# Kernel optimization log

Measured on AMD Instinct MI355X. Metric: run time of the kernel, lower is better.

## Reference

```python
import jax, jax.numpy as jnp
import numpy as np

B, D, S, H = 16384, 512, 3, 8
HD = D // H


def setup_inputs() -> dict:
    key = jax.random.key(0)
    ks = jax.random.split(key, 12)
    n = lambda k, shp, s=0.02: jax.random.normal(k, shp, jnp.float32) * s
    return {
        'x': jax.random.normal(ks[0], (B, D), jnp.float32),
        'h_prev': jax.random.normal(ks[1], (S, B, D), jnp.float32),
        'c_prev': jax.random.normal(ks[2], (S, B, D), jnp.float32),
        'ssm_state': jax.random.normal(ks[3], (B, D), jnp.float32),
        'Wt': n(ks[4], (S, D, D)),          # per-scale transform Linear weight
        'bt': jnp.zeros((S, D), jnp.float32),
        'ln_g': jnp.ones((S, D), jnp.float32),
        'ln_b': jnp.zeros((S, D), jnp.float32),
        'W_ih': n(ks[5], (S, 4 * D, D)),    # LSTMCell input weights (i,f,g,o)
        'W_hh': n(ks[6], (S, 4 * D, D)),
        'b_ih': jnp.zeros((S, 4 * D), jnp.float32),
        'b_hh': jnp.zeros((S, 4 * D), jnp.float32),
        'decays': jnp.linspace(0.5, 0.9, S, dtype=jnp.float32),
        'in_proj_w': n(ks[7], (3 * D, D)),  # MHA packed q/k/v projections
        'in_proj_b': jnp.zeros((3 * D,), jnp.float32),
        'out_proj_w': n(ks[8], (D, D)),
        'out_proj_b': jnp.zeros((D,), jnp.float32),
        'mix_w': n(ks[9], (D, S * D)),
        'mix_b': jnp.zeros((D,), jnp.float32),
    }


def reference(x, h_prev, c_prev, ssm_state, Wt, bt, ln_g, ln_b,
              W_ih, W_hh, b_ih, b_hh, decays,
              in_proj_w, in_proj_b, out_proj_w, out_proj_b, mix_w, mix_b):
    # per-scale transform: Linear -> LayerNorm -> exact GELU  (S,B,D)
    xs = jnp.einsum('bd,sed->sbe', x, Wt) + bt[:, None, :]
    mu = xs.mean(-1, keepdims=True)
    var = ((xs - mu) ** 2).mean(-1, keepdims=True)
    xs = (xs - mu) * jax.lax.rsqrt(var + 1e-5) * ln_g[:, None, :] + ln_b[:, None, :]
    xs = jax.nn.gelu(xs, approximate=False)
    # LSTMCell (all scales vectorized); gate order i,f,g,o as in torch
    gates = (jnp.einsum('sbe,sge->sbg', xs, W_ih) + b_ih[:, None, :]
             + jnp.einsum('sbd,sgd->sbg', h_prev, W_hh) + b_hh[:, None, :])
    ig, fg, gg, og = jnp.split(gates, 4, axis=-1)
    c_lstm = jax.nn.sigmoid(fg) * c_prev + jax.nn.sigmoid(ig) * jnp.tanh(gg)
    h_new = jax.nn.sigmoid(og) * jnp.tanh(c_lstm)
    d = decays[:, None, None]
    c_new = d * c_prev + (1.0 - d) * c_lstm  # decay blend (h uses pre-blend c)
    # torch.cat(outputs, dim=-1): scale-major feature blocks  (B, S*D)
    multi = jnp.transpose(h_new, (1, 0, 2)).reshape(B, S * D)
    # MHA fusion: query = ssm_state (1 token), keys/values = scale outputs
    Wq, Wk, Wv = jnp.split(in_proj_w, 3, axis=0)
    bq, bk, bv = jnp.split(in_proj_b, 3)
    q = (ssm_state @ Wq.T + bq).reshape(B, H, HD)
    k = (jnp.einsum('sbd,ed->sbe', h_new, Wk) + bk).reshape(S, B, H, HD)
    v = (jnp.einsum('sbd,ed->sbe', h_new, Wv) + bv).reshape(S, B, H, HD)
    scale = jnp.float32(1.0 / np.sqrt(HD))
    attn = jax.nn.softmax(jnp.einsum('bhd,sbhd->bhs', q, k) * scale, axis=-1)
    fused = jnp.einsum('bhs,sbhd->bhd', attn, v).reshape(B, D) @ out_proj_w.T + out_proj_b
    out = multi @ mix_w.T + mix_b + fused
    return out, h_new, c_new
```

## Files before the change

### kernel.cpp

```cpp
#include <hip/hip_runtime.h>
#include <stdint.h>


#define Bq 16384
#define Dq 512
#define Sq 3
#define Hq 8

typedef unsigned short u16;
typedef __bf16 bf16x8 __attribute__((ext_vector_type(8)));
typedef float f32x4 __attribute__((ext_vector_type(4)));
typedef u16 u16x8 __attribute__((ext_vector_type(8)));
typedef u16 u16x4v __attribute__((ext_vector_type(4)));

__device__ __forceinline__ u16 f2bf(float f) {
    union { float f; uint32_t u; } c; c.f = f;
    uint32_t u = c.u;
    return (u16)((u + 0x7fffu + ((u >> 16) & 1u)) >> 16);
}
__device__ __forceinline__ float bf2f(u16 h) {
    union { uint32_t u; float f; } c; c.u = ((uint32_t)h) << 16;
    return c.f;
}

__device__ __forceinline__ void async16(const u16* g, u16* l) {
    __builtin_amdgcn_global_load_lds(
        (__attribute__((address_space(1))) void*)const_cast<u16*>(g),
        (__attribute__((address_space(3))) void*)l, 16, 0, 0);
}

__global__ __launch_bounds__(256) void cvt_kernel(const float* __restrict__ in,
                                                  u16* __restrict__ out, long long n)
{
    long long i = ((long long)blockIdx.x * 256 + threadIdx.x) * 4;
    if (i >= n) return;
    float4 v = *(const float4*)(in + i);
    u16x4v o; o[0] = f2bf(v.x); o[1] = f2bf(v.y); o[2] = f2bf(v.z); o[3] = f2bf(v.w);
    *(u16x4v*)(out + i) = o;
}

struct Seg {
    const u16* A; long long Az; int lda;
    const u16* W; long long Wz; int ldw;
};

template<int NSEG, int OUTBF>
__global__ __launch_bounds__(256, 2)
void gemm_seg_kernel(Seg s0, Seg s1, Seg s2, Seg s3,
                     const float* __restrict__ bias0, long long b0z,
                     const float* __restrict__ bias1,
                     void* __restrict__ outp, long long outz, int ldo)
{
    __shared__ u16 As[128 * 64];
    __shared__ u16 Bs[128 * 64];
    const int tid  = threadIdx.x;
    const int lane = tid & 63;
    const int wv   = tid >> 6;
    const int wm   = wv >> 1, wn = wv & 1;
    const int z    = blockIdx.z;
    const long long rowBase = (long long)blockIdx.y * 128;
    const long long colBase = (long long)blockIdx.x * 128;

    f32x4 acc[4][4];
#pragma unroll
    for (int a = 0; a < 4; ++a)
#pragma unroll
        for (int b = 0; b < 4; ++b) acc[a][b] = (f32x4){0.f, 0.f, 0.f, 0.f};

    const int srow  = tid >> 3;
    const int scol  = (tid & 7) << 3;
    const int lrow  = lane & 15;
    const int lquad = lane >> 4;

    const Seg segs[4] = {s0, s1, s2, s3};

#pragma unroll
    for (int sg = 0; sg < NSEG; ++sg) {
        const int lda = segs[sg].lda, ldw = segs[sg].ldw;
        const u16* Ab = segs[sg].A + (long long)z * segs[sg].Az
                        + (rowBase + srow) * (long long)lda + scol;
        const u16* Wb = segs[sg].W + (long long)z * segs[sg].Wz
                        + (colBase + srow) * (long long)ldw + scol;
        for (int kt = 0; kt < 512; kt += 64) {
#pragma unroll
            for (int i = 0; i < 4; ++i) {
                async16(Ab + (long long)(i * 32) * lda + kt, &As[(i * 32 + srow) * 64 + scol]);
                async16(Wb + (long long)(i * 32) * ldw + kt, &Bs[(i * 32 + srow) * 64 + scol]);
            }
            __syncthreads();
#pragma unroll
            for (int kk = 0; kk < 64; kk += 32) {
                bf16x8 af[4], bw[4];
#pragma unroll
                for (int t = 0; t < 4; ++t)
                    af[t] = *(const bf16x8*)&As[(wm * 64 + t * 16 + lrow) * 64 + kk + lquad * 8];
#pragma unroll
                for (int t = 0; t < 4; ++t)
                    bw[t] = *(const bf16x8*)&Bs[(wn * 64 + t * 16 + lrow) * 64 + kk + lquad * 8];
#pragma unroll
                for (int mt = 0; mt < 4; ++mt)
#pragma unroll
                    for (int nt = 0; nt < 4; ++nt)
                        acc[mt][nt] = __builtin_amdgcn_mfma_f32_16x16x32_bf16(
                            af[mt], bw[nt], acc[mt][nt], 0, 0, 0);
            }
            __syncthreads();
        }
    }

#pragma unroll
    for (int nt = 0; nt < 4; ++nt) {
        const long long col = colBase + wn * 64 + nt * 16 + lrow;
        float bvv = bias0[z * b0z + col];
        if (bias1) bvv += bias1[col];
#pragma unroll
        for (int mt = 0; mt < 4; ++mt) {
            const long long row0 = rowBase + wm * 64 + mt * 16 + lquad * 4;
#pragma unroll
            for (int r = 0; r < 4; ++r) {
                const float val = acc[mt][nt][r] + bvv;
                const long long o = z * outz + (row0 + r) * (long long)ldo + col;
                if (OUTBF) ((u16*)outp)[o] = f2bf(val);
                else       ((float*)outp)[o] = val;
            }
        }
    }
}

__global__ __launch_bounds__(256) void ln_gelu_kernel(u16* __restrict__ xs,
                                                      const float* __restrict__ ln_g,
                                                      const float* __restrict__ ln_b)
{
    const int lane = threadIdx.x & 63;
    const int wvi  = threadIdx.x >> 6;
    const long long row = (long long)blockIdx.x * 4 + wvi;
    const int s = (int)(row / Bq);
    u16* p = xs + row * Dq + lane * 8;
    u16x8 u = *(const u16x8*)p;
    float v[8];
    float sum = 0.f, sq = 0.f;
#pragma unroll
    for (int j = 0; j < 8; ++j) { v[j] = bf2f(u[j]); sum += v[j]; sq += v[j] * v[j]; }
#pragma unroll
    for (int m = 32; m >= 1; m >>= 1) { sum += __shfl_xor(sum, m, 64); sq += __shfl_xor(sq, m, 64); }
    const float mu   = sum * (1.f / 512.f);
    const float var  = sq * (1.f / 512.f) - mu * mu;
    const float rstd = rsqrtf(var + 1e-5f);
    const float* g = ln_g + (size_t)s * Dq + lane * 8;
    const float* b = ln_b + (size_t)s * Dq + lane * 8;
    u16x8 o;
#pragma unroll
    for (int j = 0; j < 8; ++j) {
        float y  = (v[j] - mu) * rstd * g[j] + b[j];
        float ge = 0.5f * y * (1.f + erff(y * 0.70710678118654752f));
        o[j] = f2bf(ge);
    }
    *(u16x8*)p = o;
}

__global__ __launch_bounds__(256) void lstm_kernel(const u16* __restrict__ gates,
                                                   const float* __restrict__ cprev,
                                                   const float* __restrict__ decays, int s,
                                                   float* __restrict__ hout,
                                                   float* __restrict__ cout,
                                                   u16* __restrict__ hbf)
{
    const long long i = ((long long)blockIdx.x * 256 + threadIdx.x) * 4;
    const long long bi = i >> 9;
    const int d = (int)(i & 511);
    const u16* g = gates + bi * 2048 + d;
    u16x4v ig = *(const u16x4v*)(g);
    u16x4v fg = *(const u16x4v*)(g + 512);
    u16x4v gg = *(const u16x4v*)(g + 1024);
    u16x4v og = *(const u16x4v*)(g + 1536);
    float4 cp4 = *(const float4*)(cprev + i);
    float cpa[4] = {cp4.x, cp4.y, cp4.z, cp4.w};
    const float dec = decays[s];
    float hv[4], cv[4]; u16x4v hb;
#pragma unroll
    for (int j = 0; j < 4; ++j) {
        float igf = 1.f / (1.f + expf(-bf2f(ig[j])));
        float fgf = 1.f / (1.f + expf(-bf2f(fg[j])));
        float ggf = tanhf(bf2f(gg[j]));
        float ogf = 1.f / (1.f + expf(-bf2f(og[j])));
        float cl  = fgf * cpa[j] + igf * ggf;
        float hn  = ogf * tanhf(cl);
        hv[j] = hn;
        cv[j] = dec * cpa[j] + (1.f - dec) * cl;
        hb[j] = f2bf(hn);
    }
    *(float4*)(hout + i) = make_float4(hv[0], hv[1], hv[2], hv[3]);
    *(float4*)(cout + i) = make_float4(cv[0], cv[1], cv[2], cv[3]);
    *(u16x4v*)(hbf + i)  = hb;
}

__global__ __launch_bounds__(256) void attn_kernel(const u16* __restrict__ q,
                                                   const u16* __restrict__ k,
                                                   const u16* __restrict__ v,
                                                   u16* __restrict__ fused)
{
    const int lane = threadIdx.x & 63;
    const int wvi  = threadIdx.x >> 6;
    const long long idx = (long long)blockIdx.x * 4 + wvi;
    const long long off = idx * 64 + lane;
    const float qv = bf2f(q[off]);
    float sc[3];
#pragma unroll
    for (int s = 0; s < 3; ++s) {
        float p = qv * bf2f(k[(long long)s * Bq * Dq + off]);
#pragma unroll
        for (int m = 32; m >= 1; m >>= 1) p += __shfl_xor(p, m, 64);
        sc[s] = p * 0.125f;
    }
    const float mx = fmaxf(sc[0], fmaxf(sc[1], sc[2]));
    const float e0 = expf(sc[0] - mx), e1 = expf(sc[1] - mx), e2 = expf(sc[2] - mx);
    const float inv = 1.f / (e0 + e1 + e2);
    const float f = (e0 * bf2f(v[off]) +
                     e1 * bf2f(v[(long long)Bq * Dq + off]) +
                     e2 * bf2f(v[2LL * Bq * Dq + off])) * inv;
    fused[off] = f2bf(f);
}

extern "C" void kernel_launch(void* const* d_in, const int* in_sizes, int n_in,
                              void* d_out, int out_size, void* d_ws, size_t ws_size,
                              hipStream_t stream)
{
    (void)in_sizes; (void)n_in; (void)out_size; (void)ws_size;

    const float* x         = (const float*)d_in[0];
    const float* h_prev    = (const float*)d_in[1];
    const float* c_prev    = (const float*)d_in[2];
    const float* ssm       = (const float*)d_in[3];
    const float* Wt        = (const float*)d_in[4];
    const float* bt        = (const float*)d_in[5];
    const float* ln_g      = (const float*)d_in[6];
    const float* ln_b      = (const float*)d_in[7];
    const float* W_ih      = (const float*)d_in[8];
    const float* W_hh      = (const float*)d_in[9];
    const float* b_ih      = (const float*)d_in[10];
    const float* b_hh      = (const float*)d_in[11];
    const float* decays    = (const float*)d_in[12];
    const float* in_proj_w = (const float*)d_in[13];
    const float* in_proj_b = (const float*)d_in[14];
    const float* out_proj_w= (const float*)d_in[15];
    const float* out_proj_b= (const float*)d_in[16];
    const float* mix_w     = (const float*)d_in[17];
    const float* mix_b     = (const float*)d_in[18];
    float* out = (float*)d_out;

    u16* base = (u16*)d_ws;
    size_t off = 0;
    auto walloc = [&](size_t n) { u16* p = base + off; off += (n + 4095) & ~(size_t)4095; return p; };
    u16* wt_bf    = walloc((size_t)Sq * Dq * Dq);
    u16* wih_bf   = walloc((size_t)Sq * 4 * Dq * Dq);
    u16* whh_bf   = walloc((size_t)Sq * 4 * Dq * Dq);
    u16* inpj_bf  = walloc((size_t)3 * Dq * Dq);
    u16* outpj_bf = walloc((size_t)Dq * Dq);
    u16* mix_bf   = walloc((size_t)Dq * Sq * Dq);
    u16* x_bf     = walloc((size_t)Bq * Dq);
    u16* ssm_bf   = walloc((size_t)Bq * Dq);
    u16* hprev_bf = walloc((size_t)Sq * Bq * Dq);
    u16* xs_bf    = walloc((size_t)Sq * Bq * Dq);
    u16* gates_bf = walloc((size_t)Bq * 4 * Dq);
    u16* hnew_bf  = walloc((size_t)Sq * Bq * Dq);
    u16* k_bf = xs_bf;
    u16* v_bf = hprev_bf;
    u16* q_bf = gates_bf;
    u16* fu_bf = gates_bf + (size_t)Bq * Dq;

    auto cvt = [&](const float* s, u16* dst, long long n) {
        cvt_kernel<<<dim3((unsigned)((n / 4 + 255) / 256)), 256, 0, stream>>>(s, dst, n);
    };
    cvt(x,          x_bf,     (long long)Bq * Dq);
    cvt(ssm,        ssm_bf,   (long long)Bq * Dq);
    cvt(h_prev,     hprev_bf, (long long)Sq * Bq * Dq);
    cvt(Wt,         wt_bf,    (long long)Sq * Dq * Dq);
    cvt(W_ih,       wih_bf,   (long long)Sq * 4 * Dq * Dq);
    cvt(W_hh,       whh_bf,   (long long)Sq * 4 * Dq * Dq);
    cvt(in_proj_w,  inpj_bf,  (long long)3 * Dq * Dq);
    cvt(out_proj_w, outpj_bf, (long long)Dq * Dq);
    cvt(mix_w,      mix_bf,   (long long)Dq * Sq * Dq);

    Seg zs{nullptr, 0, 0, nullptr, 0, 0};

    {
        Seg a{x_bf, 0, Dq, wt_bf, (long long)Dq * Dq, Dq};
        gemm_seg_kernel<1, 1><<<dim3(Dq / 128, Bq / 128, Sq), 256, 0, stream>>>(
            a, zs, zs, zs, bt, Dq, nullptr, xs_bf, (long long)Bq * Dq, Dq);
    }
    ln_gelu_kernel<<<dim3(Sq * Bq / 4), 256, 0, stream>>>(xs_bf, ln_g, ln_b);

    for (int s = 0; s < Sq; ++s) {
        Seg a{xs_bf + (size_t)s * Bq * Dq, 0, Dq, wih_bf + (size_t)s * 4 * Dq * Dq, 0, Dq};
        Seg b{hprev_bf + (size_t)s * Bq * Dq, 0, Dq, whh_bf + (size_t)s * 4 * Dq * Dq, 0, Dq};
        gemm_seg_kernel<2, 1><<<dim3(4 * Dq / 128, Bq / 128, 1), 256, 0, stream>>>(
            a, b, zs, zs, b_ih + (size_t)s * 4 * Dq, 0, b_hh + (size_t)s * 4 * Dq,
            gates_bf, 0, 4 * Dq);
        lstm_kernel<<<dim3(Bq * Dq / 1024), 256, 0, stream>>>(
            gates_bf, c_prev + (size_t)s * Bq * Dq, decays, s,
            out + (size_t)Bq * Dq + (size_t)s * Bq * Dq,
            out + (size_t)4 * Bq * Dq + (size_t)s * Bq * Dq,
            hnew_bf + (size_t)s * Bq * Dq);
    }

    {
        Seg a{ssm_bf, 0, Dq, inpj_bf, 0, Dq};
        gemm_seg_kernel<1, 1><<<dim3(Dq / 128, Bq / 128, 1), 256, 0, stream>>>(
            a, zs, zs, zs, in_proj_b, 0, nullptr, q_bf, 0, Dq);
    }
    {
        Seg a{hnew_bf, (long long)Bq * Dq, Dq, inpj_bf + (size_t)Dq * Dq, 0, Dq};
        gemm_seg_kernel<1, 1><<<dim3(Dq / 128, Bq / 128, Sq), 256, 0, stream>>>(
            a, zs, zs, zs, in_proj_b + Dq, 0, nullptr, k_bf, (long long)Bq * Dq, Dq);
    }
    {
        Seg a{hnew_bf, (long long)Bq * Dq, Dq, inpj_bf + (size_t)2 * Dq * Dq, 0, Dq};
        gemm_seg_kernel<1, 1><<<dim3(Dq / 128, Bq / 128, Sq), 256, 0, stream>>>(
            a, zs, zs, zs, in_proj_b + 2 * Dq, 0, nullptr, v_bf, (long long)Bq * Dq, Dq);
    }

    attn_kernel<<<dim3(Bq * Hq / 4), 256, 0, stream>>>(q_bf, k_bf, v_bf, fu_bf);

    {
        Seg a0{hnew_bf, 0, Dq, mix_bf, 0, Sq * Dq};
        Seg a1{hnew_bf + (size_t)Bq * Dq, 0, Dq, mix_bf + Dq, 0, Sq * Dq};
        Seg a2{hnew_bf + (size_t)2 * Bq * Dq, 0, Dq, mix_bf + 2 * Dq, 0, Sq * Dq};
        Seg a3{fu_bf, 0, Dq, outpj_bf, 0, Dq};
        gemm_seg_kernel<4, 0><<<dim3(Dq / 128, Bq / 128, 1), 256, 0, stream>>>(
            a0, a1, a2, a3, mix_b, 0, out_proj_b, out, 0, Dq);
    }
}
```

Before: 1.118 ms.

## Swizzle LDS tiles, batch LSTM scales, merge conversions and QKV GEMMs into single launches

Applies an XOR swizzle to the LDS layout of the GEMM tiles to cut bank conflicts on the MFMA fragment reads. The nine fp32-to-bf16 conversions become one launch, the per-scale LSTM GEMM and cell kernels are batched across scales via grid z, and the Q/K/V projections are merged into one 7-slice GEMM launch. This removes launch overhead and tail effects from small grids. In exchange the gates buffer triples in size, and the LDS swizzle must match between the global-to-LDS writes and the fragment reads.

After: 1.017 ms. 1.1x faster.

```diff
diff --git a/kernel.cpp b/kernel.cpp
--- a/kernel.cpp
+++ b/kernel.cpp
@@ -29,27 +29,37 @@
         (__attribute__((address_space(3))) void*)l, 16, 0, 0);
 }
 
-__global__ __launch_bounds__(256) void cvt_kernel(const float* __restrict__ in,
-                                                  u16* __restrict__ out, long long n)
+struct CvtArgs {
+    const float* src[9];
+    u16* dst[9];
+    long long bound[9];
+};
+
+__global__ __launch_bounds__(256) void cvt_all_kernel(CvtArgs a, long long total)
 {
     long long i = ((long long)blockIdx.x * 256 + threadIdx.x) * 4;
-    if (i >= n) return;
-    float4 v = *(const float4*)(in + i);
+    if (i >= total) return;
+    const float* s = a.src[0];
+    u16* d = a.dst[0];
+    long long base = 0;
+#pragma unroll
+    for (int t = 0; t < 8; ++t) {
+        if (i >= a.bound[t]) { s = a.src[t + 1]; d = a.dst[t + 1]; base = a.bound[t]; }
+    }
+    const long long l = i - base;
+    float4 v = *(const float4*)(s + l);
     u16x4v o; o[0] = f2bf(v.x); o[1] = f2bf(v.y); o[2] = f2bf(v.z); o[3] = f2bf(v.w);
-    *(u16x4v*)(out + i) = o;
-}
-
-struct Seg {
-    const u16* A; long long Az; int lda;
-    const u16* W; long long Wz; int ldw;
-};
+    *(u16x4v*)(d + l) = o;
+}
+
+struct SegR { const u16* A; int lda; const u16* W; int ldw; };
+struct Seg  { const u16* A; long long Az; int lda; const u16* W; long long Wz; int ldw; };
 
 template<int NSEG, int OUTBF>
-__global__ __launch_bounds__(256, 2)
-void gemm_seg_kernel(Seg s0, Seg s1, Seg s2, Seg s3,
-                     const float* __restrict__ bias0, long long b0z,
-                     const float* __restrict__ bias1,
-                     void* __restrict__ outp, long long outz, int ldo)
+__device__ __forceinline__ void gemm_core(const SegR* segs,
+                                          const float* __restrict__ bias0,
+                                          const float* __restrict__ bias1,
+                                          void* __restrict__ outp, int ldo)
 {
     __shared__ u16 As[128 * 64];
     __shared__ u16 Bs[128 * 64];
@@ -57,7 +67,6 @@
     const int lane = tid & 63;
     const int wv   = tid >> 6;
     const int wm   = wv >> 1, wn = wv & 1;
-    const int z    = blockIdx.z;
     const long long rowBase = (long long)blockIdx.y * 128;
     const long long colBase = (long long)blockIdx.x * 128;
 
@@ -68,35 +77,33 @@
         for (int b = 0; b < 4; ++b) acc[a][b] = (f32x4){0.f, 0.f, 0.f, 0.f};
 
     const int srow  = tid >> 3;
-    const int scol  = (tid & 7) << 3;
+    const int swcol = (((tid & 7) ^ (srow & 7)) << 3);
+    const int dcol  = (tid & 7) << 3;
     const int lrow  = lane & 15;
     const int lquad = lane >> 4;
 
-    const Seg segs[4] = {s0, s1, s2, s3};
-
 #pragma unroll
     for (int sg = 0; sg < NSEG; ++sg) {
         const int lda = segs[sg].lda, ldw = segs[sg].ldw;
-        const u16* Ab = segs[sg].A + (long long)z * segs[sg].Az
-                        + (rowBase + srow) * (long long)lda + scol;
-        const u16* Wb = segs[sg].W + (long long)z * segs[sg].Wz
-                        + (colBase + srow) * (long long)ldw + scol;
+        const u16* Ab = segs[sg].A + (rowBase + srow) * (long long)lda + swcol;
+        const u16* Wb = segs[sg].W + (colBase + srow) * (long long)ldw + swcol;
         for (int kt = 0; kt < 512; kt += 64) {
 #pragma unroll
             for (int i = 0; i < 4; ++i) {
-                async16(Ab + (long long)(i * 32) * lda + kt, &As[(i * 32 + srow) * 64 + scol]);
-                async16(Wb + (long long)(i * 32) * ldw + kt, &Bs[(i * 32 + srow) * 64 + scol]);
+                async16(Ab + (long long)(i * 32) * lda + kt, &As[(i * 32 + srow) * 64 + dcol]);
+                async16(Wb + (long long)(i * 32) * ldw + kt, &Bs[(i * 32 + srow) * 64 + dcol]);
             }
             __syncthreads();
 #pragma unroll
             for (int kk = 0; kk < 64; kk += 32) {
+                const int ca = ((((kk >> 3) + lquad) ^ (lrow & 7)) << 3);
                 bf16x8 af[4], bw[4];
 #pragma unroll
                 for (int t = 0; t < 4; ++t)
-                    af[t] = *(const bf16x8*)&As[(wm * 64 + t * 16 + lrow) * 64 + kk + lquad * 8];
+                    af[t] = *(const bf16x8*)&As[(wm * 64 + t * 16 + lrow) * 64 + ca];
 #pragma unroll
                 for (int t = 0; t < 4; ++t)
-                    bw[t] = *(const bf16x8*)&Bs[(wn * 64 + t * 16 + lrow) * 64 + kk + lquad * 8];
+                    bw[t] = *(const bf16x8*)&Bs[(wn * 64 + t * 16 + lrow) * 64 + ca];
 #pragma unroll
                 for (int mt = 0; mt < 4; ++mt)
 #pragma unroll
@@ -111,7 +118,7 @@
 #pragma unroll
     for (int nt = 0; nt < 4; ++nt) {
         const long long col = colBase + wn * 64 + nt * 16 + lrow;
-        float bvv = bias0[z * b0z + col];
+        float bvv = bias0[col];
         if (bias1) bvv += bias1[col];
 #pragma unroll
         for (int mt = 0; mt < 4; ++mt) {
@@ -119,7 +126,7 @@
 #pragma unroll
             for (int r = 0; r < 4; ++r) {
                 const float val = acc[mt][nt][r] + bvv;
-                const long long o = z * outz + (row0 + r) * (long long)ldo + col;
+                const long long o = (row0 + r) * (long long)ldo + col;
                 if (OUTBF) ((u16*)outp)[o] = f2bf(val);
                 else       ((float*)outp)[o] = val;
             }
@@ -127,6 +134,56 @@
     }
 }
 
+template<int NSEG, int OUTBF>
+__global__ __launch_bounds__(256, 2)
+void gemm_seg_kernel(Seg s0, Seg s1, Seg s2, Seg s3,
+                     const float* bias0, long long b0z,
+                     const float* bias1, long long b1z,
+                     void* outp, long long outz, int ldo)
+{
+    const int z = blockIdx.z;
+    const Seg segsIn[4] = {s0, s1, s2, s3};
+    SegR segs[NSEG];
+#pragma unroll
+    for (int i = 0; i < NSEG; ++i) {
+        segs[i].A   = segsIn[i].A + (long long)z * segsIn[i].Az;
+        segs[i].lda = segsIn[i].lda;
+        segs[i].W   = segsIn[i].W + (long long)z * segsIn[i].Wz;
+        segs[i].ldw = segsIn[i].ldw;
+    }
+    gemm_core<NSEG, OUTBF>(segs,
+        bias0 + (long long)z * b0z,
+        bias1 ? bias1 + (long long)z * b1z : nullptr,
+        OUTBF ? (void*)((u16*)outp + (long long)z * outz)
+              : (void*)((float*)outp + (long long)z * outz),
+        ldo);
+}
+
+__global__ __launch_bounds__(256, 2)
+void qkv_gemm_kernel(const u16* __restrict__ hnew, const u16* __restrict__ ssm,
+                     const u16* __restrict__ inpj, const float* __restrict__ ipb,
+                     u16* __restrict__ kout, u16* __restrict__ vout,
+                     u16* __restrict__ qout)
+{
+    const int z = blockIdx.z;
+    const long long BD = (long long)Bq * Dq;
+    SegR seg[1];
+    const float* bias;
+    u16* out;
+    if (z < 3) {
+        seg[0].A = hnew + z * BD;        seg[0].W = inpj + Dq * Dq;
+        bias = ipb + Dq;                 out = kout + z * BD;
+    } else if (z < 6) {
+        seg[0].A = hnew + (z - 3) * BD;  seg[0].W = inpj + 2 * Dq * Dq;
+        bias = ipb + 2 * Dq;             out = vout + (z - 3) * BD;
+    } else {
+        seg[0].A = ssm;                  seg[0].W = inpj;
+        bias = ipb;                      out = qout;
+    }
+    seg[0].lda = Dq; seg[0].ldw = Dq;
+    gemm_core<1, 1>(seg, bias, nullptr, out, Dq);
+}
+
 __global__ __launch_bounds__(256) void ln_gelu_kernel(u16* __restrict__ xs,
                                                       const float* __restrict__ ln_g,
                                                       const float* __restrict__ ln_b)
@@ -134,7 +191,7 @@
     const int lane = threadIdx.x & 63;
     const int wvi  = threadIdx.x >> 6;
     const long long row = (long long)blockIdx.x * 4 + wvi;
-    const int s = (int)(row / Bq);
+    const int s = (int)(row >> 14);
     u16* p = xs + row * Dq + lane * 8;
     u16x8 u = *(const u16x8*)p;
     float v[8];
@@ -158,17 +215,19 @@
     *(u16x8*)p = o;
 }
 
-__global__ __launch_bounds__(256) void lstm_kernel(const u16* __restrict__ gates,
+__global__ __launch_bounds__(256) void lstm_kernel(const u16* __restrict__ gates_all,
                                                    const float* __restrict__ cprev,
-                                                   const float* __restrict__ decays, int s,
+                                                   const float* __restrict__ decays,
                                                    float* __restrict__ hout,
                                                    float* __restrict__ cout,
                                                    u16* __restrict__ hbf)
 {
     const long long i = ((long long)blockIdx.x * 256 + threadIdx.x) * 4;
-    const long long bi = i >> 9;
-    const int d = (int)(i & 511);
-    const u16* g = gates + bi * 2048 + d;
+    const int s = (int)(i >> 23);
+    const long long off = i & ((1LL << 23) - 1);
+    const long long bi = off >> 9;
+    const int d = (int)(off & 511);
+    const u16* g = gates_all + ((long long)s << 25) + bi * 2048 + d;
     u16x4v ig = *(const u16x4v*)(g);
     u16x4v fg = *(const u16x4v*)(g + 512);
     u16x4v gg = *(const u16x4v*)(g + 1024);
@@ -248,6 +307,8 @@
     const float* mix_b     = (const float*)d_in[18];
     float* out = (float*)d_out;
 
+    const long long BD = (long long)Bq * Dq;
+
     u16* base = (u16*)d_ws;
     size_t off = 0;
     auto walloc = [&](size_t n) { u16* p = base + off; off += (n + 4095) & ~(size_t)4095; return p; };
@@ -261,72 +322,58 @@
     u16* ssm_bf   = walloc((size_t)Bq * Dq);
     u16* hprev_bf = walloc((size_t)Sq * Bq * Dq);
     u16* xs_bf    = walloc((size_t)Sq * Bq * Dq);
-    u16* gates_bf = walloc((size_t)Bq * 4 * Dq);
+    u16* gates_bf = walloc((size_t)Sq * Bq * 4 * Dq);
     u16* hnew_bf  = walloc((size_t)Sq * Bq * Dq);
-    u16* k_bf = xs_bf;
-    u16* v_bf = hprev_bf;
-    u16* q_bf = gates_bf;
-    u16* fu_bf = gates_bf + (size_t)Bq * Dq;
-
-    auto cvt = [&](const float* s, u16* dst, long long n) {
-        cvt_kernel<<<dim3((unsigned)((n / 4 + 255) / 256)), 256, 0, stream>>>(s, dst, n);
-    };
-    cvt(x,          x_bf,     (long long)Bq * Dq);
-    cvt(ssm,        ssm_bf,   (long long)Bq * Dq);
-    cvt(h_prev,     hprev_bf, (long long)Sq * Bq * Dq);
-    cvt(Wt,         wt_bf,    (long long)Sq * Dq * Dq);
-    cvt(W_ih,       wih_bf,   (long long)Sq * 4 * Dq * Dq);
-    cvt(W_hh,       whh_bf,   (long long)Sq * 4 * Dq * Dq);
-    cvt(in_proj_w,  inpj_bf,  (long long)3 * Dq * Dq);
-    cvt(out_proj_w, outpj_bf, (long long)Dq * Dq);
-    cvt(mix_w,      mix_bf,   (long long)Dq * Sq * Dq);
+    u16* k_bf  = xs_bf;
+    u16* v_bf  = hprev_bf;
+    u16* q_bf  = gates_bf;
+    u16* fu_bf = gates_bf + BD;
+
+    {
+        CvtArgs a;
+        const float* srcs[9] = {x, ssm, h_prev, Wt, W_ih, W_hh, in_proj_w, out_proj_w, mix_w};
+        u16* dsts[9] = {x_bf, ssm_bf, hprev_bf, wt_bf, wih_bf, whh_bf, inpj_bf, outpj_bf, mix_bf};
+        const long long ns[9] = {BD, BD, Sq * BD,
+                                 (long long)Sq * Dq * Dq, (long long)Sq * 4 * Dq * Dq,
+                                 (long long)Sq * 4 * Dq * Dq, (long long)3 * Dq * Dq,
+                                 (long long)Dq * Dq, (long long)Dq * Sq * Dq};
+        long long acc = 0;
+        for (int i = 0; i < 9; ++i) { a.src[i] = srcs[i]; a.dst[i] = dsts[i]; acc += ns[i]; a.bound[i] = acc; }
+        cvt_all_kernel<<<dim3((unsigned)((acc / 4 + 255) / 256)), 256, 0, stream>>>(a, acc);
+    }
 
     Seg zs{nullptr, 0, 0, nullptr, 0, 0};
 
     {
         Seg a{x_bf, 0, Dq, wt_bf, (long long)Dq * Dq, Dq};
         gemm_seg_kernel<1, 1><<<dim3(Dq / 128, Bq / 128, Sq), 256, 0, stream>>>(
-            a, zs, zs, zs, bt, Dq, nullptr, xs_bf, (long long)Bq * Dq, Dq);
+            a, zs, zs, zs, bt, Dq, nullptr, 0, xs_bf, BD, Dq);
     }
     ln_gelu_kernel<<<dim3(Sq * Bq / 4), 256, 0, stream>>>(xs_bf, ln_g, ln_b);
 
-    for (int s = 0; s < Sq; ++s) {
-        Seg a{xs_bf + (size_t)s * Bq * Dq, 0, Dq, wih_bf + (size_t)s * 4 * Dq * Dq, 0, Dq};
-        Seg b{hprev_bf + (size_t)s * Bq * Dq, 0, Dq, whh_bf + (size_t)s * 4 * Dq * Dq, 0, Dq};
-        gemm_seg_kernel<2, 1><<<dim3(4 * Dq / 128, Bq / 128, 1), 256, 0, stream>>>(
-            a, b, zs, zs, b_ih + (size_t)s * 4 * Dq, 0, b_hh + (size_t)s * 4 * Dq,
-            gates_bf, 0, 4 * Dq);
-        lstm_kernel<<<dim3(Bq * Dq / 1024), 256, 0, stream>>>(
-            gates_bf, c_prev + (size_t)s * Bq * Dq, decays, s,
-            out + (size_t)Bq * Dq + (size_t)s * Bq * Dq,
-            out + (size_t)4 * Bq * Dq + (size_t)s * Bq * Dq,
-            hnew_bf + (size_t)s * Bq * Dq);
-    }
-
     {
-        Seg a{ssm_bf, 0, Dq, inpj_bf, 0, Dq};
-        gemm_seg_kernel<1, 1><<<dim3(Dq / 128, Bq / 128, 1), 256, 0, stream>>>(
-            a, zs, zs, zs, in_proj_b, 0, nullptr, q_bf, 0, Dq);
-    }
-    {
-        Seg a{hnew_bf, (long long)Bq * Dq, Dq, inpj_bf + (size_t)Dq * Dq, 0, Dq};
-        gemm_seg_kernel<1, 1><<<dim3(Dq / 128, Bq / 128, Sq), 256, 0, stream>>>(
-            a, zs, zs, zs, in_proj_b + Dq, 0, nullptr, k_bf, (long long)Bq * Dq, Dq);
-    }
-    {
-        Seg a{hnew_bf, (long long)Bq * Dq, Dq, inpj_bf + (size_t)2 * Dq * Dq, 0, Dq};
-        gemm_seg_kernel<1, 1><<<dim3(Dq / 128, Bq / 128, Sq), 256, 0, stream>>>(
-            a, zs, zs, zs, in_proj_b + 2 * Dq, 0, nullptr, v_bf, (long long)Bq * Dq, Dq);
-    }
+        Seg a{xs_bf, BD, Dq, wih_bf, (long long)4 * Dq * Dq, Dq};
+        Seg b{hprev_bf, BD, Dq, whh_bf, (long long)4 * Dq * Dq, Dq};
+        gemm_seg_kernel<2, 1><<<dim3(4 * Dq / 128, Bq / 128, Sq), 256, 0, stream>>>(
+            a, b, zs, zs, b_ih, 4 * Dq, b_hh, 4 * Dq, gates_bf, 4 * BD, 4 * Dq);
+    }
+    lstm_kernel<<<dim3(Sq * Bq * Dq / 1024), 256, 0, stream>>>(
+        gates_bf, c_prev, decays,
+        out + BD,
+        out + 4 * BD,
+        hnew_bf);
+
+    qkv_gemm_kernel<<<dim3(Dq / 128, Bq / 128, 7), 256, 0, stream>>>(
+        hnew_bf, ssm_bf, inpj_bf, in_proj_b, k_bf, v_bf, q_bf);
 
     attn_kernel<<<dim3(Bq * Hq / 4), 256, 0, stream>>>(q_bf, k_bf, v_bf, fu_bf);
 
     {
         Seg a0{hnew_bf, 0, Dq, mix_bf, 0, Sq * Dq};
-        Seg a1{hnew_bf + (size_t)Bq * Dq, 0, Dq, mix_bf + Dq, 0, Sq * Dq};
-        Seg a2{hnew_bf + (size_t)2 * Bq * Dq, 0, Dq, mix_bf + 2 * Dq, 0, Sq * Dq};
+        Seg a1{hnew_bf + BD, 0, Dq, mix_bf + Dq, 0, Sq * Dq};
+        Seg a2{hnew_bf + 2 * BD, 0, Dq, mix_bf + 2 * Dq, 0, Sq * Dq};
         Seg a3{fu_bf, 0, Dq, outpj_bf, 0, Dq};
         gemm_seg_kernel<4, 0><<<dim3(Dq / 128, Bq / 128, 1), 256, 0, stream>>>(
-            a0, a1, a2, a3, mix_b, 0, out_proj_b, out, 0, Dq);
-    }
-}
+            a0, a1, a2, a3, mix_b, 0, out_proj_b, 0, out, 0, Dq);
+    }
+}
```
